# Optimization experiments

Hardware: AMD Instinct MI355X
Metric: run time of the kernel (lower is better)

## Reference

```python
import jax, jax.numpy as jnp
import numpy as np

D_MODEL = 1024
NUM_HEADS = 16
HEAD_DIM = D_MODEL // NUM_HEADS
SEQ_LEN = 2048
THETA = 10000.0


def setup_inputs() -> dict:
    key = jax.random.key(0)
    ks = jax.random.split(key, 9)
    s = 1.0 / np.sqrt(D_MODEL)
    inp = {
        "x": jax.random.normal(ks[0], (2, SEQ_LEN, D_MODEL), dtype=jnp.float32),
        "Wq": jax.random.uniform(ks[1], (D_MODEL, D_MODEL), jnp.float32, -s, s),
        "bq": jax.random.uniform(ks[2], (D_MODEL,), jnp.float32, -s, s),
        "Wk": jax.random.uniform(ks[3], (D_MODEL, D_MODEL), jnp.float32, -s, s),
        "bk": jax.random.uniform(ks[4], (D_MODEL,), jnp.float32, -s, s),
        "Wv": jax.random.uniform(ks[5], (D_MODEL, D_MODEL), jnp.float32, -s, s),
        "bv": jax.random.uniform(ks[6], (D_MODEL,), jnp.float32, -s, s),
        "Wo": jax.random.uniform(ks[7], (D_MODEL, D_MODEL), jnp.float32, -s, s),
        "bo": jax.random.uniform(ks[8], (D_MODEL,), jnp.float32, -s, s),
    }
    return inp


def _rope_cos_sin(seq_len, dim, theta):
    inv_freq = 1.0 / theta ** (jnp.arange(0, dim, 2, dtype=jnp.float32) / dim)  # [dim/2]
    t = jnp.arange(seq_len, dtype=jnp.float32)
    freqs = jnp.outer(t, inv_freq)  # [S, dim/2]
    return jnp.cos(freqs), jnp.sin(freqs)


def _apply_rope(x, cos, sin):
    # x: [B, H, S, head_dim]; interleaved complex pairs (even, odd)
    x2 = x.reshape(*x.shape[:-1], -1, 2)  # [B,H,S,hd/2,2]
    xe, xo = x2[..., 0], x2[..., 1]
    c = cos[None, None, :, :]
    s = sin[None, None, :, :]
    oe = xe * c - xo * s
    oo = xe * s + xo * c
    return jnp.stack([oe, oo], axis=-1).reshape(x.shape)


def reference(x, Wq, bq, Wk, bk, Wv, bv, Wo, bo):
    B, S, D = x.shape
    H, hd = NUM_HEADS, HEAD_DIM
    q = x @ Wq.T + bq
    k = x @ Wk.T + bk
    v = x @ Wv.T + bv
    # [B, H, S, hd]
    q = q.reshape(B, S, H, hd).transpose(0, 2, 1, 3)
    k = k.reshape(B, S, H, hd).transpose(0, 2, 1, 3)
    v = v.reshape(B, S, H, hd).transpose(0, 2, 1, 3)
    cos, sin = _rope_cos_sin(S, hd, THETA)
    q = _apply_rope(q, cos, sin)
    k = _apply_rope(k, cos, sin)
    scores = jnp.einsum("bhqd,bhkd->bhqk", q, k) / jnp.sqrt(jnp.float32(hd))
    causal = jnp.triu(jnp.ones((S, S), dtype=bool), k=1)
    scores = jnp.where(causal[None, None, :, :], -jnp.inf, scores)
    attn = jax.nn.softmax(scores, axis=-1)
    out = jnp.einsum("bhqk,bhkd->bhqd", attn, v)
    out = out.transpose(0, 2, 1, 3).reshape(B, S, D)
    return out @ Wo.T + bo
```

## Files before the change

kernel.cpp:

```cpp
#include <hip/hip_runtime.h>
#include <hip/hip_bf16.h>

#define S_LEN 2048
#define DM 1024
#define NH 16
#define HD 64
#define M_ROWS 4096
#define LOG2E 1.4426950408889634f
#define MASKVAL -1.0e4f
#define QSCALE 0.18033688011112042f

typedef __attribute__((ext_vector_type(8))) short short8;
typedef __attribute__((ext_vector_type(2))) float f32x2;
typedef __attribute__((ext_vector_type(4))) float f32x4;
typedef __attribute__((ext_vector_type(16))) float f32x16;

__device__ inline ushort f2b(float f) {
  union { float f; unsigned u; } v; v.f = f;
  unsigned r = v.u + 0x7fffu + ((v.u >> 16) & 1u);
  return (ushort)(r >> 16);
}

__device__ inline float b2f(ushort u) {
  union { unsigned u; float f; } v; v.u = ((unsigned)u) << 16; return v.f;
}

__device__ inline unsigned pk_bf16(float a, float b) {
  __hip_bfloat162 h = __float22bfloat162_rn(make_float2(a, b));
  union { __hip_bfloat162 h; unsigned u; } v; v.h = h;
  return v.u;
}

__device__ inline float fexp2(float x) { return __builtin_amdgcn_exp2f(x); }

__device__ inline void gl_lds16(const void* g, void* l) {
  __builtin_amdgcn_global_load_lds(
      (const __attribute__((address_space(1))) void*)g,
      (__attribute__((address_space(3))) void*)l, 16, 0, 0);
}

__global__ __launch_bounds__(256) void cast_rope_kernel(
    const float* __restrict__ x, const float* __restrict__ Wq, const float* __restrict__ Wk,
    const float* __restrict__ Wv, const float* __restrict__ Wo,
    ushort* __restrict__ xb, ushort* __restrict__ Wqb, ushort* __restrict__ Wkb,
    ushort* __restrict__ Wvb, ushort* __restrict__ Wob,
    float* __restrict__ ropeC, float* __restrict__ ropeS) {
  const int bid = blockIdx.x;
  if (bid >= 8192) {
    int idx = (bid - 8192) * 256 + threadIdx.x;
    int s = idx >> 5, i = idx & 31;
    float inv = exp2f(-(float)i * (13.287712379549449f / 32.0f));
    float a = (float)s * inv;
    ropeC[idx] = cosf(a);
    ropeS[idx] = sinf(a);
    return;
  }
  int i = bid * 256 + threadIdx.x;
  int r = i >> 18, off = i & 0x3FFFF;
  const float4* s;
  uint2* d;
  switch (r) {
    case 0: case 1: case 2: case 3: s = (const float4*)x + i;  d = (uint2*)xb + i;  break;
    case 4: s = (const float4*)Wq + off; d = (uint2*)Wqb + off; break;
    case 5: s = (const float4*)Wk + off; d = (uint2*)Wkb + off; break;
    case 6: s = (const float4*)Wv + off; d = (uint2*)Wvb + off; break;
    default: s = (const float4*)Wo + off; d = (uint2*)Wob + off; break;
  }
  float4 v = *s;
  uint2 o;
  o.x = pk_bf16(v.x, v.y);
  o.y = pk_bf16(v.z, v.w);
  *d = o;
}

__global__ __launch_bounds__(256) void gemm_qkv_kernel(const ushort* __restrict__ xb,
    const ushort* __restrict__ Wqb, const ushort* __restrict__ Wkb, const ushort* __restrict__ Wvb,
    const float* __restrict__ bq, const float* __restrict__ bk, const float* __restrict__ bv,
    const float* __restrict__ ropeC, const float* __restrict__ ropeS,
    ushort* __restrict__ qb, ushort* __restrict__ kb, ushort* __restrict__ vT) {
  __shared__ ushort lds[24576];
  const int lid = blockIdx.x;
  const int xcd = lid & 7;
  const int idx = lid >> 3;
  const int z = idx >> 5;
  const int rem = idx & 31;
  const int mi = ((xcd & 3) << 3) | (rem & 7);
  const int ni = ((xcd >> 2) << 2) | (rem >> 3);
  const int m0 = mi * 128, n0 = ni * 128;
  const ushort* W = (z == 0) ? Wqb : ((z == 1) ? Wkb : Wvb);
  const float* bias = (z == 0) ? bq : ((z == 1) ? bk : bv);
  const int t = threadIdx.x, lane = t & 63, wave = t >> 6;
  const int wr = (wave >> 1) * 64, wc = (wave & 1) * 64;
  const int lr = lane & 15, lg = lane >> 4;

  const int slot0 = wave * 128 + lane, slot1 = slot0 + 64;
  const int row0 = slot0 >> 2, g0 = (slot0 & 3) ^ (row0 & 3);
  const int row1 = slot1 >> 2, g1 = (slot1 & 3) ^ (row1 & 3);
  const ushort* Ap0 = &xb[(size_t)(m0 + row0) * DM + g0 * 8];
  const ushort* Ap1 = &xb[(size_t)(m0 + row1) * DM + g1 * 8];
  const ushort* Wp0 = &W[(size_t)(n0 + row0) * DM + g0 * 8];
  const ushort* Wp1 = &W[(size_t)(n0 + row1) * DM + g1 * 8];

  f32x4 acc[4][4];
#pragma unroll
  for (int a = 0; a < 4; a++)
#pragma unroll
    for (int b = 0; b < 4; b++) acc[a][b] = (f32x4){0.f, 0.f, 0.f, 0.f};

  gl_lds16(Ap0, &lds[slot0 * 8]);
  gl_lds16(Ap1, &lds[slot1 * 8]);
  gl_lds16(Wp0, &lds[12288 + slot0 * 8]);
  gl_lds16(Wp1, &lds[12288 + slot1 * 8]);
  gl_lds16(Ap0 + 32, &lds[4096 + slot0 * 8]);
  gl_lds16(Ap1 + 32, &lds[4096 + slot1 * 8]);
  gl_lds16(Wp0 + 32, &lds[16384 + slot0 * 8]);
  gl_lds16(Wp1 + 32, &lds[16384 + slot1 * 8]);
  asm volatile("s_waitcnt vmcnt(4)" ::: "memory");
  __builtin_amdgcn_s_barrier();
  __builtin_amdgcn_sched_barrier(0);

  int cur = 0;
  for (int i = 0; i < 32; i++) {
    const bool pref = (i + 2 < 32);
    if (pref) {
      const int nb = (cur >= 1) ? cur - 1 : 2;
      const int k0 = (i + 2) * 32;
      gl_lds16(Ap0 + k0, &lds[nb * 4096 + slot0 * 8]);
      gl_lds16(Ap1 + k0, &lds[nb * 4096 + slot1 * 8]);
      gl_lds16(Wp0 + k0, &lds[12288 + nb * 4096 + slot0 * 8]);
      gl_lds16(Wp1 + k0, &lds[12288 + nb * 4096 + slot1 * 8]);
    }
    const int fb = cur * 4096;
    short8 af[4], bf[4];
#pragma unroll
    for (int mt = 0; mt < 4; mt++) {
      const int row = wr + mt * 16 + lr;
      af[mt] = *(const short8*)&lds[fb + (row * 4 + (lg ^ (row & 3))) * 8];
    }
#pragma unroll
    for (int nt = 0; nt < 4; nt++) {
      const int row = wc + nt * 16 + lr;
      bf[nt] = *(const short8*)&lds[12288 + fb + (row * 4 + (lg ^ (row & 3))) * 8];
    }
#pragma unroll
    for (int mt = 0; mt < 4; mt++)
#pragma unroll
      for (int nt = 0; nt < 4; nt++)
        acc[mt][nt] = __builtin_amdgcn_mfma_f32_16x16x32_bf16(af[mt], bf[nt], acc[mt][nt], 0, 0, 0);
    if (i + 1 < 32) {
      if (pref) asm volatile("s_waitcnt vmcnt(4)" ::: "memory");
      else      asm volatile("s_waitcnt vmcnt(0)" ::: "memory");
      __builtin_amdgcn_s_barrier();
      __builtin_amdgcn_sched_barrier(0);
    }
    cur = (cur >= 2) ? 0 : cur + 1;
  }
  __syncthreads();

#pragma unroll
  for (int mt = 0; mt < 4; mt++) {
#pragma unroll
    for (int nt = 0; nt < 4; nt++) {
      const int nloc = wc + nt * 16 + lr;
      const float bn = bias[n0 + nloc];
#pragma unroll
      for (int r = 0; r < 4; r++) {
        const int mloc = wr + mt * 16 + lg * 4 + r;
        const ushort v = f2b(acc[mt][nt][r] + bn);
        if (z < 2) lds[mloc * 136 + nloc] = v;
        else       lds[nloc * 136 + mloc] = v;
      }
    }
  }
  __syncthreads();

  const int b = m0 >> 11;
  if (z < 2) {
    ushort* dst = (z == 0) ? qb : kb;
    const float qscale = (z == 0) ? QSCALE : 1.0f;
#pragma unroll
    for (int c = 0; c < 8; c++) {
      const int sloc = c * 16 + (t >> 4);
      const int nloc = (t & 15) * 8;
      short8 val = *(const short8*)&lds[sloc * 136 + nloc];
      const int s = (m0 + sloc) & (S_LEN - 1);
      const int h = (n0 + nloc) >> 6;
      const int d0 = nloc & 63;
      const float4 cv = *(const float4*)&ropeC[s * 32 + d0 / 2];
      const float4 sv = *(const float4*)&ropeS[s * 32 + d0 / 2];
      uint4 o;
      {
        float e = b2f((ushort)val[0]), od = b2f((ushort)val[1]);
        o.x = pk_bf16((e * cv.x - od * sv.x) * qscale, (e * sv.x + od * cv.x) * qscale);
      }
      {
        float e = b2f((ushort)val[2]), od = b2f((ushort)val[3]);
        o.y = pk_bf16((e * cv.y - od * sv.y) * qscale, (e * sv.y + od * cv.y) * qscale);
      }
      {
        float e = b2f((ushort)val[4]), od = b2f((ushort)val[5]);
        o.z = pk_bf16((e * cv.z - od * sv.z) * qscale, (e * sv.z + od * cv.z) * qscale);
      }
      {
        float e = b2f((ushort)val[6]), od = b2f((ushort)val[7]);
        o.w = pk_bf16((e * cv.w - od * sv.w) * qscale, (e * sv.w + od * cv.w) * qscale);
      }
      *(uint4*)&dst[(((size_t)b * NH + h) * S_LEN + s) * HD + d0] = o;
    }
  } else {
    const int sbase = m0 & (S_LEN - 1);
#pragma unroll
    for (int c = 0; c < 8; c++) {
      const int nloc = c * 16 + (t >> 4);
      const int s0 = (t & 15) * 8;
      short8 val = *(const short8*)&lds[nloc * 136 + s0];
      const int h = (n0 + nloc) >> 6;
      const int d = nloc & 63;
      *(short8*)&vT[(((size_t)b * NH + h) * HD + d) * S_LEN + sbase + s0] = val;
    }
  }
}

__global__ __launch_bounds__(256) void flash_kernel(const ushort* __restrict__ qb,
                                                    const ushort* __restrict__ kb,
                                                    const ushort* __restrict__ vT,
                                                    ushort* __restrict__ attn) {
  __shared__ ushort lds[32768];
  const int t = threadIdx.x, lane = t & 63, wave = t >> 6;
  const int q31 = lane & 31, h = lane >> 5;
  const int lid = blockIdx.x;
  const int g = lid >> 5;
  const int qt = (g < 8) ? (15 - g) : (g - 8);
  const int bh = lid & 31;
  const int q0 = qt * 128;
  const int nint = qt + 1;

  const ushort* kbh = kb + (size_t)bh * S_LEN * HD;
  const ushort* vbh = vT + (size_t)bh * HD * S_LEN;

  const int qrow = q0 + wave * 32 + q31;
  const ushort* qptr = qb + ((size_t)bh * S_LEN + qrow) * HD + h * 8;
  short8 qf[4];
#pragma unroll
  for (int s = 0; s < 4; s++) qf[s] = *(const short8*)(qptr + s * 16);

  const int slot0 = wave * 128 + lane, slot1 = slot0 + 64;
  const int row0 = slot0 >> 3, g0 = (slot0 & 7) ^ (row0 & 7);
  const int row1 = slot1 >> 3, g1 = (slot1 & 7) ^ (row1 & 7);
  const int lo0 = wave * 128 * 8, lo1 = lo0 + 64 * 8;

  int foff[4][2];
#pragma unroll
  for (int s = 0; s < 4; s++)
#pragma unroll
    for (int st = 0; st < 2; st++) {
      const int row = st * 32 + q31;
      foff[s][st] = (row * 8 + ((2 * s + h) ^ (row & 7))) * 8;
    }

  const ushort* kp0 = kbh + (size_t)row0 * HD + g0 * 8;
  const ushort* kp1 = kbh + (size_t)row1 * HD + g1 * 8;
  const ushort* vp0 = vbh + (size_t)row0 * S_LEN + g0 * 8;
  const ushort* vp1 = vbh + (size_t)row1 * S_LEN + g1 * 8;

#pragma unroll
  for (int ha = 0; ha < 2; ++ha) {
    gl_lds16(kp0, &lds[ha * 4096 + lo0]);
    gl_lds16(kp1, &lds[ha * 4096 + lo1]);
    gl_lds16(vp0, &lds[16384 + ha * 4096 + lo0]);
    gl_lds16(vp1, &lds[16384 + ha * 4096 + lo1]);
    kp0 += 64 * HD; kp1 += 64 * HD; vp0 += 64; vp1 += 64;
  }

  f32x16 O[2];
#pragma unroll
  for (int st = 0; st < 2; st++)
#pragma unroll
    for (int r = 0; r < 16; r++) O[st][r] = 0.f;

  f32x16 zc;
#pragma unroll
  for (int r = 0; r < 16; r++) zc[r] = 0.f;

  f32x2 lpA = (f32x2){0.f, 0.f}, lpB = (f32x2){0.f, 0.f};

  asm volatile("s_waitcnt vmcnt(0)" ::: "memory");
  __builtin_amdgcn_s_barrier();
  __builtin_amdgcn_sched_barrier(0);

  int buf = 0;
  for (int j = 0; j < nint; ++j) {
    const bool pref = (j + 1 < nint);
    if (pref) {
      const int nb = (buf ^ 1) * 8192;
#pragma unroll
      for (int ha = 0; ha < 2; ++ha) {
        gl_lds16(kp0, &lds[nb + ha * 4096 + lo0]);
        gl_lds16(kp1, &lds[nb + ha * 4096 + lo1]);
        gl_lds16(vp0, &lds[16384 + nb + ha * 4096 + lo0]);
        gl_lds16(vp1, &lds[16384 + nb + ha * 4096 + lo1]);
        kp0 += 64 * HD; kp1 += 64 * HD; vp0 += 64; vp1 += 64;
      }
    }

#pragma unroll
    for (int ha = 0; ha < 2; ++ha) {
      const ushort* Kb = &lds[buf * 8192 + ha * 4096];
      const ushort* Vb = &lds[16384 + buf * 8192 + ha * 4096];
      const int kt = 2 * j + ha;

      f32x16 sc0, sc1;
      __builtin_amdgcn_s_setprio(1);
      sc0 = __builtin_amdgcn_mfma_f32_32x32x16_bf16(
          *(const short8*)&Kb[foff[0][0]], qf[0], zc, 0, 0, 0);
      sc1 = __builtin_amdgcn_mfma_f32_32x32x16_bf16(
          *(const short8*)&Kb[foff[0][1]], qf[0], zc, 0, 0, 0);
#pragma unroll
      for (int s = 1; s < 4; s++) {
        sc0 = __builtin_amdgcn_mfma_f32_32x32x16_bf16(
            *(const short8*)&Kb[foff[s][0]], qf[s], sc0, 0, 0, 0);
        sc1 = __builtin_amdgcn_mfma_f32_32x32x16_bf16(
            *(const short8*)&Kb[foff[s][1]], qf[s], sc1, 0, 0, 0);
      }
      __builtin_amdgcn_s_setprio(0);

      if (kt * 64 + 63 > q0 + wave * 32) {
#pragma unroll
        for (int r = 0; r < 16; r++) {
          const int kc0 = kt * 64 + (r & 3) + 8 * (r >> 2) + 4 * h;
          if (kc0 > qrow) sc0[r] = MASKVAL;
          if (kc0 + 32 > qrow) sc1[r] = MASKVAL;
        }
      }
#pragma unroll
      for (int r = 0; r < 16; r += 2) {
        const float a0 = fexp2(sc0[r]), a1 = fexp2(sc0[r + 1]);
        const float b0 = fexp2(sc1[r]), b1 = fexp2(sc1[r + 1]);
        sc0[r] = a0; sc0[r + 1] = a1;
        sc1[r] = b0; sc1[r + 1] = b1;
        lpA += (f32x2){a0, a1};
        lpB += (f32x2){b0, b1};
      }

      unsigned pp[8][2];
#pragma unroll
      for (int rg = 0; rg < 4; rg++) {
        pp[rg][0] = pk_bf16(sc0[4 * rg + 0], sc0[4 * rg + 1]);
        pp[rg][1] = pk_bf16(sc0[4 * rg + 2], sc0[4 * rg + 3]);
        pp[4 + rg][0] = pk_bf16(sc1[4 * rg + 0], sc1[4 * rg + 1]);
        pp[4 + rg][1] = pk_bf16(sc1[4 * rg + 2], sc1[4 * rg + 3]);
      }
      __builtin_amdgcn_s_setprio(1);
#pragma unroll
      for (int s = 0; s < 4; s++) {
        unsigned d0 = pp[2 * s][0], e0 = pp[2 * s + 1][0];
        unsigned d1 = pp[2 * s][1], e1 = pp[2 * s + 1][1];
        asm("v_permlane32_swap_b32 %0, %1" : "+v"(d0), "+v"(e0));
        asm("v_permlane32_swap_b32 %0, %1" : "+v"(d1), "+v"(e1));
        union { unsigned u[4]; short8 v; } pf;
        pf.u[0] = d0;
        pf.u[1] = d1;
        pf.u[2] = e0;
        pf.u[3] = e1;
        O[0] = __builtin_amdgcn_mfma_f32_32x32x16_bf16(
            *(const short8*)&Vb[foff[s][0]], pf.v, O[0], 0, 0, 0);
        O[1] = __builtin_amdgcn_mfma_f32_32x32x16_bf16(
            *(const short8*)&Vb[foff[s][1]], pf.v, O[1], 0, 0, 0);
      }
      __builtin_amdgcn_s_setprio(0);
    }

    if (pref) {
      asm volatile("s_waitcnt vmcnt(0)" ::: "memory");
      __builtin_amdgcn_s_barrier();
      __builtin_amdgcn_sched_barrier(0);
    }
    buf ^= 1;
  }

  float lacc = (lpA[0] + lpA[1]) + (lpB[0] + lpB[1]);
  lacc += __shfl_xor(lacc, 32);
  const float inv = 1.f / lacc;

  const int b = bh >> 4, hh = bh & 15;
  const int q = q0 + wave * 32 + q31;
  ushort* obase = attn + ((size_t)b * S_LEN + q) * DM + hh * HD;
#pragma unroll
  for (int st = 0; st < 2; st++)
#pragma unroll
    for (int rg = 0; rg < 4; rg++) {
      const int d0 = st * 32 + 8 * rg + 4 * h;
      uint2 w;
      w.x = pk_bf16(O[st][4 * rg + 0] * inv, O[st][4 * rg + 1] * inv);
      w.y = pk_bf16(O[st][4 * rg + 2] * inv, O[st][4 * rg + 3] * inv);
      *(uint2*)&obase[d0] = w;
    }
}

__global__ __launch_bounds__(256) void gemm_out_kernel(const ushort* __restrict__ attn,
                                                       const ushort* __restrict__ Wob,
                                                       const float* __restrict__ bo,
                                                       float* __restrict__ out) {
  __shared__ ushort lds[18432];
  const int lid = blockIdx.x;
  const int xcd = lid & 7;
  const int idx = lid >> 3;
  const int mi = ((xcd & 3) << 3) | (idx & 7);
  const int ni = ((xcd >> 2) << 3) | (idx >> 3);
  const int m0 = mi * 128, n0 = ni * 64;
  const int t = threadIdx.x, lane = t & 63, wave = t >> 6;
  const int wm = (wave >> 1) * 64, wn = (wave & 1) * 32;
  const int lr = lane & 15, lg = lane >> 4;
  const int slotA0 = wave * 128 + lane, slotA1 = slotA0 + 64;
  const int rowA0 = slotA0 >> 2, gA0 = (slotA0 & 3) ^ (rowA0 & 3);
  const int rowA1 = slotA1 >> 2, gA1 = (slotA1 & 3) ^ (rowA1 & 3);
  const int slotB = wave * 64 + lane;
  const int rowB = slotB >> 2, gB = (slotB & 3) ^ (rowB & 3);
  const ushort* Ap0 = &attn[(size_t)(m0 + rowA0) * DM + gA0 * 8];
  const ushort* Ap1 = &attn[(size_t)(m0 + rowA1) * DM + gA1 * 8];
  const ushort* Wp  = &Wob[(size_t)(n0 + rowB) * DM + gB * 8];

  f32x4 acc[4][2];
#pragma unroll
  for (int a = 0; a < 4; a++)
#pragma unroll
    for (int b = 0; b < 2; b++) acc[a][b] = (f32x4){0.f, 0.f, 0.f, 0.f};

  gl_lds16(Ap0, &lds[slotA0 * 8]);
  gl_lds16(Ap1, &lds[slotA1 * 8]);
  gl_lds16(Wp, &lds[12288 + slotB * 8]);
  gl_lds16(Ap0 + 32, &lds[4096 + slotA0 * 8]);
  gl_lds16(Ap1 + 32, &lds[4096 + slotA1 * 8]);
  gl_lds16(Wp + 32, &lds[14336 + slotB * 8]);
  asm volatile("s_waitcnt vmcnt(3)" ::: "memory");
  __builtin_amdgcn_s_barrier();
  __builtin_amdgcn_sched_barrier(0);

  int cur = 0;
  for (int i = 0; i < 32; i++) {
    const bool pref = (i + 2 < 32);
    if (pref) {
      const int nb = (cur >= 1) ? cur - 1 : 2;
      const int k0 = (i + 2) * 32;
      gl_lds16(Ap0 + k0, &lds[nb * 4096 + slotA0 * 8]);
      gl_lds16(Ap1 + k0, &lds[nb * 4096 + slotA1 * 8]);
      gl_lds16(Wp + k0, &lds[12288 + nb * 2048 + slotB * 8]);
    }
    short8 af[4], bf[2];
#pragma unroll
    for (int mt = 0; mt < 4; mt++) {
      const int row = wm + mt * 16 + lr;
      af[mt] = *(const short8*)&lds[cur * 4096 + (row * 4 + (lg ^ (row & 3))) * 8];
    }
#pragma unroll
    for (int nt = 0; nt < 2; nt++) {
      const int row = wn + nt * 16 + lr;
      bf[nt] = *(const short8*)&lds[12288 + cur * 2048 + (row * 4 + (lg ^ (row & 3))) * 8];
    }
#pragma unroll
    for (int mt = 0; mt < 4; mt++)
#pragma unroll
      for (int nt = 0; nt < 2; nt++)
        acc[mt][nt] = __builtin_amdgcn_mfma_f32_16x16x32_bf16(af[mt], bf[nt], acc[mt][nt], 0, 0, 0);
    if (i + 1 < 32) {
      if (pref) asm volatile("s_waitcnt vmcnt(3)" ::: "memory");
      else      asm volatile("s_waitcnt vmcnt(0)" ::: "memory");
      __builtin_amdgcn_s_barrier();
      __builtin_amdgcn_sched_barrier(0);
    }
    cur = (cur >= 2) ? 0 : cur + 1;
  }

#pragma unroll
  for (int mt = 0; mt < 4; mt++) {
#pragma unroll
    for (int nt = 0; nt < 2; nt++) {
      const int n = n0 + wn + nt * 16 + lr;
      const float bn = bo[n];
#pragma unroll
      for (int r = 0; r < 4; r++) {
        const int m = m0 + wm + mt * 16 + lg * 4 + r;
        out[(size_t)m * DM + n] = acc[mt][nt][r] + bn;
      }
    }
  }
}

extern "C" void kernel_launch(void* const* d_in, const int* in_sizes, int n_in,
                              void* d_out, int out_size, void* d_ws, size_t ws_size,
                              hipStream_t stream) {
  const float* x  = (const float*)d_in[0];
  const float* Wq = (const float*)d_in[1];
  const float* bq = (const float*)d_in[2];
  const float* Wk = (const float*)d_in[3];
  const float* bk = (const float*)d_in[4];
  const float* Wv = (const float*)d_in[5];
  const float* bv = (const float*)d_in[6];
  const float* Wo = (const float*)d_in[7];
  const float* bo = (const float*)d_in[8];
  float* out = (float*)d_out;

  char* ws = (char*)d_ws;
  size_t off = 0;
  auto alloc = [&](size_t bytes) { char* p = ws + off; off += (bytes + 255) & ~255ull; return p; };
  ushort* xb   = (ushort*)alloc((size_t)M_ROWS * DM * 2);
  ushort* Wqb  = (ushort*)alloc((size_t)DM * DM * 2);
  ushort* Wkb  = (ushort*)alloc((size_t)DM * DM * 2);
  ushort* Wvb  = (ushort*)alloc((size_t)DM * DM * 2);
  ushort* Wob  = (ushort*)alloc((size_t)DM * DM * 2);
  ushort* qb   = (ushort*)alloc((size_t)M_ROWS * DM * 2);
  ushort* kb   = (ushort*)alloc((size_t)M_ROWS * DM * 2);
  ushort* vTb  = (ushort*)alloc((size_t)M_ROWS * DM * 2);
  ushort* attn = (ushort*)alloc((size_t)M_ROWS * DM * 2);
  float* ropeC = (float*)alloc((size_t)S_LEN * 32 * 4);
  float* ropeS = (float*)alloc((size_t)S_LEN * 32 * 4);
  (void)ws_size; (void)in_sizes; (void)n_in; (void)out_size;

  cast_rope_kernel<<<8448, 256, 0, stream>>>(x, Wq, Wk, Wv, Wo, xb, Wqb, Wkb, Wvb, Wob,
                                             ropeC, ropeS);
  gemm_qkv_kernel<<<768, 256, 0, stream>>>(
      xb, Wqb, Wkb, Wvb, bq, bk, bv, ropeC, ropeS, qb, kb, vTb);
  flash_kernel<<<512, 256, 0, stream>>>(qb, kb, vTb, attn);
  gemm_out_kernel<<<512, 256, 0, stream>>>(attn, Wob, bo, out);
}
```

Baseline: 181.5 us.

## Switch projection GEMMs to double-buffered 64-wide K stages with half the barriers

The QKV and output projection GEMMs move from a three-stage ring of 32-wide K tiles (one barrier per tile) to two buffers of 64-wide K tiles, each computed as two 32-wide halves. This halves the number of barrier and wait points in the K loop. It cuts how far ahead loads are issued, since the code now waits with vmcnt(0) for the next stage right after computing the current one, and it raises LDS use per block, which may reduce occupancy.

```diff
diff --git a/kernel.cpp b/kernel.cpp
--- a/kernel.cpp
+++ b/kernel.cpp
@@ -78,7 +78,7 @@
     const float* __restrict__ bq, const float* __restrict__ bk, const float* __restrict__ bv,
     const float* __restrict__ ropeC, const float* __restrict__ ropeS,
     ushort* __restrict__ qb, ushort* __restrict__ kb, ushort* __restrict__ vT) {
-  __shared__ ushort lds[24576];
+  __shared__ ushort lds[32768];
   const int lid = blockIdx.x;
   const int xcd = lid & 7;
   const int idx = lid >> 3;
@@ -107,53 +107,58 @@
 #pragma unroll
     for (int b = 0; b < 4; b++) acc[a][b] = (f32x4){0.f, 0.f, 0.f, 0.f};
 
-  gl_lds16(Ap0, &lds[slot0 * 8]);
-  gl_lds16(Ap1, &lds[slot1 * 8]);
-  gl_lds16(Wp0, &lds[12288 + slot0 * 8]);
-  gl_lds16(Wp1, &lds[12288 + slot1 * 8]);
-  gl_lds16(Ap0 + 32, &lds[4096 + slot0 * 8]);
-  gl_lds16(Ap1 + 32, &lds[4096 + slot1 * 8]);
-  gl_lds16(Wp0 + 32, &lds[16384 + slot0 * 8]);
-  gl_lds16(Wp1 + 32, &lds[16384 + slot1 * 8]);
-  asm volatile("s_waitcnt vmcnt(4)" ::: "memory");
+#pragma unroll
+  for (int ha = 0; ha < 2; ++ha) {
+    const int k0 = ha * 32;
+    gl_lds16(Ap0 + k0, &lds[ha * 4096 + slot0 * 8]);
+    gl_lds16(Ap1 + k0, &lds[ha * 4096 + slot1 * 8]);
+    gl_lds16(Wp0 + k0, &lds[16384 + ha * 4096 + slot0 * 8]);
+    gl_lds16(Wp1 + k0, &lds[16384 + ha * 4096 + slot1 * 8]);
+  }
+  asm volatile("s_waitcnt vmcnt(0)" ::: "memory");
   __builtin_amdgcn_s_barrier();
   __builtin_amdgcn_sched_barrier(0);
 
-  int cur = 0;
-  for (int i = 0; i < 32; i++) {
-    const bool pref = (i + 2 < 32);
+  int buf = 0;
+  for (int j = 0; j < 16; ++j) {
+    const bool pref = (j + 1 < 16);
     if (pref) {
-      const int nb = (cur >= 1) ? cur - 1 : 2;
-      const int k0 = (i + 2) * 32;
-      gl_lds16(Ap0 + k0, &lds[nb * 4096 + slot0 * 8]);
-      gl_lds16(Ap1 + k0, &lds[nb * 4096 + slot1 * 8]);
-      gl_lds16(Wp0 + k0, &lds[12288 + nb * 4096 + slot0 * 8]);
-      gl_lds16(Wp1 + k0, &lds[12288 + nb * 4096 + slot1 * 8]);
-    }
-    const int fb = cur * 4096;
-    short8 af[4], bf[4];
-#pragma unroll
-    for (int mt = 0; mt < 4; mt++) {
-      const int row = wr + mt * 16 + lr;
-      af[mt] = *(const short8*)&lds[fb + (row * 4 + (lg ^ (row & 3))) * 8];
-    }
-#pragma unroll
-    for (int nt = 0; nt < 4; nt++) {
-      const int row = wc + nt * 16 + lr;
-      bf[nt] = *(const short8*)&lds[12288 + fb + (row * 4 + (lg ^ (row & 3))) * 8];
-    }
-#pragma unroll
-    for (int mt = 0; mt < 4; mt++)
-#pragma unroll
-      for (int nt = 0; nt < 4; nt++)
-        acc[mt][nt] = __builtin_amdgcn_mfma_f32_16x16x32_bf16(af[mt], bf[nt], acc[mt][nt], 0, 0, 0);
-    if (i + 1 < 32) {
-      if (pref) asm volatile("s_waitcnt vmcnt(4)" ::: "memory");
-      else      asm volatile("s_waitcnt vmcnt(0)" ::: "memory");
+      const int nb = (buf ^ 1) * 8192;
+#pragma unroll
+      for (int ha = 0; ha < 2; ++ha) {
+        const int k0 = (2 * j + 2 + ha) * 32;
+        gl_lds16(Ap0 + k0, &lds[nb + ha * 4096 + slot0 * 8]);
+        gl_lds16(Ap1 + k0, &lds[nb + ha * 4096 + slot1 * 8]);
+        gl_lds16(Wp0 + k0, &lds[16384 + nb + ha * 4096 + slot0 * 8]);
+        gl_lds16(Wp1 + k0, &lds[16384 + nb + ha * 4096 + slot1 * 8]);
+      }
+    }
+#pragma unroll
+    for (int ha = 0; ha < 2; ++ha) {
+      const int fb = buf * 8192 + ha * 4096;
+      short8 af[4], bf[4];
+#pragma unroll
+      for (int mt = 0; mt < 4; mt++) {
+        const int row = wr + mt * 16 + lr;
+        af[mt] = *(const short8*)&lds[fb + (row * 4 + (lg ^ (row & 3))) * 8];
+      }
+#pragma unroll
+      for (int nt = 0; nt < 4; nt++) {
+        const int row = wc + nt * 16 + lr;
+        bf[nt] = *(const short8*)&lds[16384 + fb + (row * 4 + (lg ^ (row & 3))) * 8];
+      }
+#pragma unroll
+      for (int mt = 0; mt < 4; mt++)
+#pragma unroll
+        for (int nt = 0; nt < 4; nt++)
+          acc[mt][nt] = __builtin_amdgcn_mfma_f32_16x16x32_bf16(af[mt], bf[nt], acc[mt][nt], 0, 0, 0);
+    }
+    if (pref) {
+      asm volatile("s_waitcnt vmcnt(0)" ::: "memory");
       __builtin_amdgcn_s_barrier();
       __builtin_amdgcn_sched_barrier(0);
     }
-    cur = (cur >= 2) ? 0 : cur + 1;
+    buf ^= 1;
   }
   __syncthreads();
 
@@ -401,7 +406,7 @@
                                                        const ushort* __restrict__ Wob,
                                                        const float* __restrict__ bo,
                                                        float* __restrict__ out) {
-  __shared__ ushort lds[18432];
+  __shared__ ushort lds[24576];
   const int lid = blockIdx.x;
   const int xcd = lid & 7;
   const int idx = lid >> 3;
@@ -426,49 +431,58 @@
 #pragma unroll
     for (int b = 0; b < 2; b++) acc[a][b] = (f32x4){0.f, 0.f, 0.f, 0.f};
 
-  gl_lds16(Ap0, &lds[slotA0 * 8]);
-  gl_lds16(Ap1, &lds[slotA1 * 8]);
-  gl_lds16(Wp, &lds[12288 + slotB * 8]);
-  gl_lds16(Ap0 + 32, &lds[4096 + slotA0 * 8]);
-  gl_lds16(Ap1 + 32, &lds[4096 + slotA1 * 8]);
-  gl_lds16(Wp + 32, &lds[14336 + slotB * 8]);
-  asm volatile("s_waitcnt vmcnt(3)" ::: "memory");
+#pragma unroll
+  for (int ha = 0; ha < 2; ++ha) {
+    const int k0 = ha * 32;
+    gl_lds16(Ap0 + k0, &lds[ha * 4096 + slotA0 * 8]);
+    gl_lds16(Ap1 + k0, &lds[ha * 4096 + slotA1 * 8]);
+    gl_lds16(Wp + k0, &lds[16384 + ha * 2048 + slotB * 8]);
+  }
+  asm volatile("s_waitcnt vmcnt(0)" ::: "memory");
   __builtin_amdgcn_s_barrier();
   __builtin_amdgcn_sched_barrier(0);
 
-  int cur = 0;
-  for (int i = 0; i < 32; i++) {
-    const bool pref = (i + 2 < 32);
+  int buf = 0;
+  for (int j = 0; j < 16; ++j) {
+    const bool pref = (j + 1 < 16);
     if (pref) {
-      const int nb = (cur >= 1) ? cur - 1 : 2;
-      const int k0 = (i + 2) * 32;
-      gl_lds16(Ap0 + k0, &lds[nb * 4096 + slotA0 * 8]);
-      gl_lds16(Ap1 + k0, &lds[nb * 4096 + slotA1 * 8]);
-      gl_lds16(Wp + k0, &lds[12288 + nb * 2048 + slotB * 8]);
-    }
-    short8 af[4], bf[2];
-#pragma unroll
-    for (int mt = 0; mt < 4; mt++) {
-      const int row = wm + mt * 16 + lr;
-      af[mt] = *(const short8*)&lds[cur * 4096 + (row * 4 + (lg ^ (row & 3))) * 8];
-    }
-#pragma unroll
-    for (int nt = 0; nt < 2; nt++) {
-      const int row = wn + nt * 16 + lr;
-      bf[nt] = *(const short8*)&lds[12288 + cur * 2048 + (row * 4 + (lg ^ (row & 3))) * 8];
-    }
-#pragma unroll
-    for (int mt = 0; mt < 4; mt++)
-#pragma unroll
-      for (int nt = 0; nt < 2; nt++)
-        acc[mt][nt] = __builtin_amdgcn_mfma_f32_16x16x32_bf16(af[mt], bf[nt], acc[mt][nt], 0, 0, 0);
-    if (i + 1 < 32) {
-      if (pref) asm volatile("s_waitcnt vmcnt(3)" ::: "memory");
-      else      asm volatile("s_waitcnt vmcnt(0)" ::: "memory");
+      const int nbA = (buf ^ 1) * 8192;
+      const int nbB = 16384 + (buf ^ 1) * 4096;
+#pragma unroll
+      for (int ha = 0; ha < 2; ++ha) {
+        const int k0 = (2 * j + 2 + ha) * 32;
+        gl_lds16(Ap0 + k0, &lds[nbA + ha * 4096 + slotA0 * 8]);
+        gl_lds16(Ap1 + k0, &lds[nbA + ha * 4096 + slotA1 * 8]);
+        gl_lds16(Wp + k0, &lds[nbB + ha * 2048 + slotB * 8]);
+      }
+    }
+#pragma unroll
+    for (int ha = 0; ha < 2; ++ha) {
+      const int fbA = buf * 8192 + ha * 4096;
+      const int fbB = 16384 + buf * 4096 + ha * 2048;
+      short8 af[4], bf[2];
+#pragma unroll
+      for (int mt = 0; mt < 4; mt++) {
+        const int row = wm + mt * 16 + lr;
+        af[mt] = *(const short8*)&lds[fbA + (row * 4 + (lg ^ (row & 3))) * 8];
+      }
+#pragma unroll
+      for (int nt = 0; nt < 2; nt++) {
+        const int row = wn + nt * 16 + lr;
+        bf[nt] = *(const short8*)&lds[fbB + (row * 4 + (lg ^ (row & 3))) * 8];
+      }
+#pragma unroll
+      for (int mt = 0; mt < 4; mt++)
+#pragma unroll
+        for (int nt = 0; nt < 2; nt++)
+          acc[mt][nt] = __builtin_amdgcn_mfma_f32_16x16x32_bf16(af[mt], bf[nt], acc[mt][nt], 0, 0, 0);
+    }
+    if (pref) {
+      asm volatile("s_waitcnt vmcnt(0)" ::: "memory");
       __builtin_amdgcn_s_barrier();
       __builtin_amdgcn_sched_barrier(0);
     }
-    cur = (cur >= 2) ? 0 : cur + 1;
+    buf ^= 1;
   }
 
 #pragma unroll
```

New measurement: 184.4 us. No clear change (+1.6%).
